# Kernel optimization log

Measured on AMD Instinct MI355X. Metric: run time of the kernel, lower is better.

The kernel has to match this reference:

```python
import jax, jax.numpy as jnp
import numpy as np

N = 4096
IN_DIM = 256
OUT_DIM = 256
E = 131072


def setup_inputs() -> dict:
    key = jax.random.key(0)
    ks = jax.random.split(key, 8)
    x = jax.random.normal(ks[0], (N, IN_DIM), dtype=jnp.float32)
    edge_index = jax.random.randint(ks[1], (2, E), 0, N, dtype=jnp.int64)
    lap = jax.random.normal(ks[2], (N, N), dtype=jnp.float32)
    d_inv = jax.random.normal(ks[3], (N, N), dtype=jnp.float32)
    # parameters
    W_high = jax.random.normal(ks[4], (IN_DIM, OUT_DIM), dtype=jnp.float32) / np.sqrt(IN_DIM)
    W_conv = jax.random.normal(ks[5], (IN_DIM, OUT_DIM), dtype=jnp.float32) / np.sqrt(IN_DIM)
    b_conv = jnp.zeros((OUT_DIM,), dtype=jnp.float32)
    aL = jax.random.uniform(ks[6], (1,), dtype=jnp.float32)
    aH = jax.random.uniform(ks[7], (1,), dtype=jnp.float32)
    return {"x": x, "edge_index": edge_index, "lap": lap, "d_inv": d_inv,
            "W_high": W_high, "W_conv": W_conv, "b_conv": b_conv,
            "aL": aL, "aH": aH}


def _gcn_conv(x, edge_index, W, b, num_nodes):
    # PyG GCNConv: add self-loops, symmetric normalization, aggregate at target.
    src, dst = edge_index[0], edge_index[1]
    loop = jnp.arange(num_nodes, dtype=edge_index.dtype)
    src_f = jnp.concatenate([src, loop])
    dst_f = jnp.concatenate([dst, loop])
    deg = jax.ops.segment_sum(jnp.ones_like(dst_f, dtype=x.dtype), dst_f,
                              num_segments=num_nodes)
    deg_inv_sqrt = jnp.where(deg > 0, jax.lax.rsqrt(jnp.maximum(deg, 1e-12)), 0.0)
    norm = deg_inv_sqrt[src_f] * deg_inv_sqrt[dst_f]  # [E+N]
    xw = x @ W                                        # [N, out]
    msgs = xw[src_f] * norm[:, None]                  # [E+N, out]
    out = jax.ops.segment_sum(msgs, dst_f, num_segments=num_nodes)
    return out + b


def reference(x, edge_index, lap, d_inv, W_high, W_conv, b_conv, aL, aH):
    # high-pass branch: Lhp = d_inv @ lap @ d_inv; Hh = Lhp @ relu(x @ W_high)
    Lhp = (d_inv @ lap) @ d_inv
    Hh = Lhp @ jax.nn.relu(x @ W_high)
    # low-pass branch: GCNConv
    Hl = _gcn_conv(x, edge_index, W_conv, b_conv, x.shape[0])
    return aL * Hl + aH * Hh
```

## Files before the change

### kernel.cpp

```cpp
#include <hip/hip_runtime.h>

#define NN 4096
#define DD 256
#define EE 131072

typedef __attribute__((ext_vector_type(8))) short s16x8;
typedef __attribute__((ext_vector_type(4))) float f32x4;

__device__ __forceinline__ unsigned short f2bf(float f) {
  unsigned u = __builtin_bit_cast(unsigned, f);
  u += 0x7FFFu + ((u >> 16) & 1u);
  return (unsigned short)(u >> 16);
}

__device__ __forceinline__ ushort4 cvt4(f32x4 v) {
  ushort4 r;
  r.x = f2bf(v[0]); r.y = f2bf(v[1]); r.z = f2bf(v[2]); r.w = f2bf(v[3]);
  return r;
}

__device__ __forceinline__ unsigned cvt2_rhu(float a, float b) {
  unsigned ua = __builtin_bit_cast(unsigned, a) + 0x8000u;
  unsigned ub = __builtin_bit_cast(unsigned, b) + 0x8000u;
  return __builtin_amdgcn_perm(ub, ua, 0x07060302u);
}

__device__ __forceinline__ uint4 pack8(f32x4 a, f32x4 b) {
  uint4 r;
  r.x = cvt2_rhu(a[0], a[1]); r.y = cvt2_rhu(a[2], a[3]);
  r.z = cvt2_rhu(b[0], b[1]); r.w = cvt2_rhu(b[2], b[3]);
  return r;
}


__global__ void k_prep(const int* __restrict__ ei, int* __restrict__ deg,
                       const float* __restrict__ Wh, const float* __restrict__ Wc,
                       unsigned short* __restrict__ WFh, unsigned short* __restrict__ WFc) {
  int t = blockIdx.x * 256 + threadIdx.x;
  if (t < EE) {
    atomicAdd(&deg[ei[EE + t]], 1);
  } else {
    int idx = t - EE;
    int which = idx >> 16;
    int r = idx & 65535;
    int n = r & 255, k = r >> 8;
    const float* W = which ? Wc : Wh;
    unsigned short* WF = which ? WFc : WFh;
    long fidx = ((long)((n >> 4) * 8 + (k >> 5))) * 512 +
                (((k >> 3) & 3) * 16 + (n & 15)) * 8 + (k & 7);
    WF[fidx] = f2bf(W[k * 256 + n]);
  }
}

__global__ void k_scan(const int* __restrict__ deg, int* __restrict__ row_start,
                       float* __restrict__ dis) {
  __shared__ int part[1024];
  int t = threadIdx.x;
  int d0 = deg[4 * t + 0], d1 = deg[4 * t + 1], d2 = deg[4 * t + 2], d3 = deg[4 * t + 3];
  int s = d0 + d1 + d2 + d3;
  part[t] = s;
  __syncthreads();
  for (int off = 1; off < 1024; off <<= 1) {
    int add = (t >= off) ? part[t - off] : 0;
    __syncthreads();
    part[t] += add;
    __syncthreads();
  }
  int base = part[t] - s;
  row_start[4 * t + 0] = base;
  row_start[4 * t + 1] = base + d0;
  row_start[4 * t + 2] = base + d0 + d1;
  row_start[4 * t + 3] = base + d0 + d1 + d2;
  if (t == 1023) row_start[4096] = part[t];
  dis[4 * t + 0] = rsqrtf((float)d0 + 1.0f);
  dis[4 * t + 1] = rsqrtf((float)d1 + 1.0f);
  dis[4 * t + 2] = rsqrtf((float)d2 + 1.0f);
  dis[4 * t + 3] = rsqrtf((float)d3 + 1.0f);
}

__global__ void k_scatter(const int* __restrict__ ei, const int* __restrict__ row_start,
                          int* __restrict__ cursor, int* __restrict__ csr) {
  int e = blockIdx.x * 256 + threadIdx.x;
  if (e < EE) {
    int s = ei[e];
    int d = ei[EE + e];
    int p = atomicAdd(&cursor[d], 1);
    csr[row_start[d] + p] = s;
  }
}

__global__ __launch_bounds__(512) void k_xw(const float* __restrict__ x,
                                            const unsigned short* __restrict__ WFh,
                                            const unsigned short* __restrict__ WFc,
                                            unsigned short* __restrict__ RF,
                                            float* __restrict__ XWs,
                                            const float* __restrict__ dis) {
  __shared__ alignas(16) unsigned short Abuf[16][264];
  const int tid = threadIdx.x;
  const int w = tid >> 6, lane = tid & 63;
  const int quad = lane >> 4, l16 = lane & 15, quad8 = quad * 8;
  const int m0 = blockIdx.x * 16;

  {
    int srow = tid >> 5, scolf = (tid & 31) * 8;
    const float* ap = x + (long)(m0 + srow) * DD + scolf;
    f32x4 a0 = *(const f32x4*)ap;
    f32x4 a1 = *(const f32x4*)(ap + 4);
    *(uint4*)&Abuf[srow][scolf] = pack8(a0, a1);
  }
  __syncthreads();

  const bool hi = (w < 4);
  const int wo = hi ? w : (w - 4);
  const unsigned short* WF = hi ? WFh : WFc;
  const unsigned short* bp = WF + lane * 8;

  f32x4 acc[4] = {{0,0,0,0},{0,0,0,0},{0,0,0,0},{0,0,0,0}};
#pragma unroll
  for (int q = 0; q < 8; ++q) {
    s16x8 af = *(const s16x8*)&Abuf[l16][q * 32 + quad8];
#pragma unroll
    for (int s = 0; s < 4; ++s) {
      s16x8 bf = *(const s16x8*)(bp + ((long)((4 * wo + s) * 8 + q)) * 512);
      acc[s] = __builtin_amdgcn_mfma_f32_16x16x32_bf16(af, bf, acc[s], 0, 0, 0);
    }
  }

  if (hi) {
    const int kc = m0 >> 5;
    const int qp = ((m0 >> 4) & 1) * 2 + (quad >> 1);
    const int j0 = (quad & 1) * 4;
#pragma unroll
    for (int s = 0; s < 4; ++s) {
      int t = 4 * wo + s;
      f32x4 v = acc[s];
      f32x4 z;
      z[0] = v[0] > 0.f ? v[0] : 0.f;
      z[1] = v[1] > 0.f ? v[1] : 0.f;
      z[2] = v[2] > 0.f ? v[2] : 0.f;
      z[3] = v[3] > 0.f ? v[3] : 0.f;
      long idx = ((long)(t * 128 + kc)) * 512 + (qp * 16 + l16) * 8 + j0;
      *(ushort4*)(RF + idx) = cvt4(z);
    }
  } else {
    float dm[4];
#pragma unroll
    for (int r = 0; r < 4; ++r) dm[r] = dis[m0 + quad * 4 + r];
#pragma unroll
    for (int s = 0; s < 4; ++s) {
      int col = 64 * wo + 16 * s + l16;
#pragma unroll
      for (int r = 0; r < 4; ++r)
        XWs[(long)(m0 + quad * 4 + r) * DD + col] = dm[r] * acc[s][r];
    }
  }
}

__global__ void k_agg(const float* __restrict__ XWs, const int* __restrict__ row_start,
                      const int* __restrict__ csr, const float* __restrict__ dis,
                      float* __restrict__ Hl) {
  const int i = blockIdx.x;
  const int t = threadIdx.x;
  const int b0 = row_start[i], b1 = row_start[i + 1];
  float acc = XWs[(long)i * DD + t];
  int j = b0;
  for (; j + 4 <= b1; j += 4) {
    int s0 = csr[j], s1 = csr[j + 1], s2 = csr[j + 2], s3 = csr[j + 3];
    float v0 = XWs[(long)s0 * DD + t];
    float v1 = XWs[(long)s1 * DD + t];
    float v2 = XWs[(long)s2 * DD + t];
    float v3 = XWs[(long)s3 * DD + t];
    acc += (v0 + v1) + (v2 + v3);
  }
  for (; j < b1; ++j) acc += XWs[(long)csr[j] * DD + t];
  Hl[(long)i * DD + t] = dis[i] * acc;
}

template <int EPI>
__global__ __launch_bounds__(512) void k_mm2(const float* __restrict__ A,
                                             const unsigned short* __restrict__ BF,
                                             unsigned short* __restrict__ CF,
                                             float* __restrict__ outF,
                                             const float* __restrict__ Hl,
                                             const float* __restrict__ bconv,
                                             const float* __restrict__ aLp,
                                             const float* __restrict__ aHp) {
  __shared__ alignas(16) unsigned short As[2][32 * 512];
  const int tid = threadIdx.x;
  const int w = tid >> 6, lane = tid & 63;
  const int quad = lane >> 4, l16 = lane & 15;
  const int mblk = blockIdx.x & 127, nhalf = blockIdx.x >> 7;
  const int msub = w & 1, nsub = w >> 1;
  const int m0 = mblk * 32;
  const int t0 = nhalf * 8 + nsub * 2;

  const int srow = tid >> 4;
  const int sg = tid & 15;
  const int sswz = srow & 7;
  const float* asrc = A + (long)(m0 + srow) * NN + sg * 8;
  unsigned short* const wbase0 = &As[0][srow * 512];
  unsigned short* const wbase1 = &As[1][srow * 512];

  const int row = msub * 16 + l16;
  const int r7 = row & 7;
  const unsigned short* const rbase0 = &As[0][row * 512];
  const unsigned short* const rbase1 = &As[1][row * 512];

  const unsigned short* bq0 = BF + ((long)t0 * 128) * 512 + lane * 8;
  const unsigned short* bq1 = bq0 + 128l * 512;

  f32x4 acc0 = {0, 0, 0, 0}, acc1 = {0, 0, 0, 0};

  {
#pragma unroll
    for (int j = 0; j < 4; ++j) {
      f32x4 lo = *(const f32x4*)(asrc + j * 128);
      f32x4 hi = *(const f32x4*)(asrc + j * 128 + 4);
      *(uint4*)(wbase0 + (((sg + 16 * j) ^ sswz) * 8)) = pack8(lo, hi);
    }
  }
  __syncthreads();

#pragma unroll 1
  for (int s = 0; s < 8; ++s) {
    f32x4 p0, p1, p2, p3, p4, p5, p6, p7;
    if (s + 1 < 8) {
      const float* ap = asrc + (s + 1) * 512;
      p0 = *(const f32x4*)(ap + 0 * 128); p1 = *(const f32x4*)(ap + 0 * 128 + 4);
      p2 = *(const f32x4*)(ap + 1 * 128); p3 = *(const f32x4*)(ap + 1 * 128 + 4);
      p4 = *(const f32x4*)(ap + 2 * 128); p5 = *(const f32x4*)(ap + 2 * 128 + 4);
      p6 = *(const f32x4*)(ap + 3 * 128); p7 = *(const f32x4*)(ap + 3 * 128 + 4);
    }
    __builtin_amdgcn_sched_barrier(0);

    const unsigned short* rb = (s & 1) ? rbase1 : rbase0;
#pragma unroll
    for (int c = 0; c < 16; ++c) {
      s16x8 af = *(const s16x8*)(rb + (((c * 4 + quad) ^ r7) * 8));
      long kb = (long)(s * 16 + c) * 512;
      s16x8 b0 = *(const s16x8*)(bq0 + kb);
      s16x8 b1 = *(const s16x8*)(bq1 + kb);
      acc0 = __builtin_amdgcn_mfma_f32_16x16x32_bf16(af, b0, acc0, 0, 0, 0);
      acc1 = __builtin_amdgcn_mfma_f32_16x16x32_bf16(af, b1, acc1, 0, 0, 0);
    }

    if (s + 1 < 8) {
      unsigned short* wb = ((s + 1) & 1) ? wbase1 : wbase0;
      *(uint4*)(wb + (((sg + 0)  ^ sswz) * 8)) = pack8(p0, p1);
      *(uint4*)(wb + (((sg + 16) ^ sswz) * 8)) = pack8(p2, p3);
      *(uint4*)(wb + (((sg + 32) ^ sswz) * 8)) = pack8(p4, p5);
      *(uint4*)(wb + (((sg + 48) ^ sswz) * 8)) = pack8(p6, p7);
    }
    __syncthreads();
  }

  if constexpr (EPI == 0) {
    const int qp = msub * 2 + (quad >> 1);
    const int j0 = (quad & 1) * 4;
    long i0 = ((long)(t0 * 128 + mblk)) * 512 + (qp * 16 + l16) * 8 + j0;
    long i1 = ((long)((t0 + 1) * 128 + mblk)) * 512 + (qp * 16 + l16) * 8 + j0;
    *(ushort4*)(CF + i0) = cvt4(acc0);
    *(ushort4*)(CF + i1) = cvt4(acc1);
  } else {
    const float aLv = aLp[0], aHv = aHp[0];
    const int mr = m0 + msub * 16 + quad * 4;
    const int c0 = t0 * 16 + l16;
    const int c1 = c0 + 16;
#pragma unroll
    for (int r = 0; r < 4; ++r) {
      int rr = mr + r;
      outF[(long)rr * DD + c0] =
          aHv * acc0[r] + aLv * (Hl[(long)rr * DD + c0] + bconv[c0]);
      outF[(long)rr * DD + c1] =
          aHv * acc1[r] + aLv * (Hl[(long)rr * DD + c1] + bconv[c1]);
    }
  }
}

extern "C" void kernel_launch(void* const* d_in, const int* in_sizes, int n_in,
                              void* d_out, int out_size, void* d_ws, size_t ws_size,
                              hipStream_t stream) {
  const float* x     = (const float*)d_in[0];
  const int*   ei    = (const int*)d_in[1];
  const float* lap   = (const float*)d_in[2];
  const float* dinv  = (const float*)d_in[3];
  const float* Wh    = (const float*)d_in[4];
  const float* Wc    = (const float*)d_in[5];
  const float* bconv = (const float*)d_in[6];
  const float* aL    = (const float*)d_in[7];
  const float* aH    = (const float*)d_in[8];
  float* out = (float*)d_out;
  char* ws = (char*)d_ws;

  int* deg        = (int*)(ws);
  int* cursor     = (int*)(ws + (16 << 10));
  int* row_start  = (int*)(ws + (32 << 10));
  int* csr        = (int*)(ws + (64 << 10));
  float* dis      = (float*)(ws + (576 << 10));
  unsigned short* WFh = (unsigned short*)(ws + (1l << 20));
  unsigned short* WFc = (unsigned short*)(ws + (1l << 20) + (128 << 10));
  unsigned short* RF  = (unsigned short*)(ws + (2l << 20));
  unsigned short* T1F = (unsigned short*)(ws + (4l << 20));
  unsigned short* T2F = (unsigned short*)(ws + (6l << 20));
  float* XWs = (float*)(ws + (8l << 20));
  float* Hl  = (float*)(ws + (12l << 20));

  hipMemsetAsync(ws, 0, 32 << 10, stream);

  k_prep<<<1024, 256, 0, stream>>>(ei, deg, Wh, Wc, WFh, WFc);
  k_scan<<<1, 1024, 0, stream>>>(deg, row_start, dis);
  k_scatter<<<512, 256, 0, stream>>>(ei, row_start, cursor, csr);
  k_xw<<<256, 512, 0, stream>>>(x, WFh, WFc, RF, XWs, dis);
  k_agg<<<4096, 256, 0, stream>>>(XWs, row_start, csr, dis, Hl);

  k_mm2<0><<<256, 512, 0, stream>>>(dinv, RF, T1F, nullptr, nullptr, nullptr, nullptr, nullptr);
  k_mm2<0><<<256, 512, 0, stream>>>(lap, T1F, T2F, nullptr, nullptr, nullptr, nullptr, nullptr);
  k_mm2<3><<<256, 512, 0, stream>>>(dinv, T2F, nullptr, out, Hl, bconv, aL, aH);
}
```

Baseline: 282.1 us.

## Split-K the big GEMMs with 128-row tiles, async LDS loads, atomic accumulation

Replaces the 32-row-tile GEMM, which read B straight from global memory, with a split-K kernel. Each block handles a 128-row tile over a 512-wide K slice and half of the N columns. A and B are staged into LDS with global_load_lds, and the fp32 A tile is converted to bf16 while building fragments. Partial results are combined with fp32 atomics into a zeroed buffer, and separate convert and finalize kernels write the bf16 fragment layout and the output epilogue. This gives more reuse per block and more parallelism, at the cost of atomic traffic, extra memsets and extra launches.

New measurement: 339.6 us. 1.2x slower.

```diff
diff --git a/kernel.cpp b/kernel.cpp
--- a/kernel.cpp
+++ b/kernel.cpp
@@ -30,6 +30,17 @@
   r.x = cvt2_rhu(a[0], a[1]); r.y = cvt2_rhu(a[2], a[3]);
   r.z = cvt2_rhu(b[0], b[1]); r.w = cvt2_rhu(b[2], b[3]);
   return r;
+}
+
+__device__ __forceinline__ s16x8 pack8f(f32x4 a, f32x4 b) {
+  uint4 p = pack8(a, b);
+  return __builtin_bit_cast(s16x8, p);
+}
+
+__device__ __forceinline__ void gl2lds(const float* g, float* l) {
+  __builtin_amdgcn_global_load_lds(
+      (const __attribute__((address_space(1))) unsigned*)g,
+      (__attribute__((address_space(3))) unsigned*)l, 16, 0, 0);
 }
 
 
@@ -176,105 +187,121 @@
   Hl[(long)i * DD + t] = dis[i] * acc;
 }
 
-template <int EPI>
-__global__ __launch_bounds__(512) void k_mm2(const float* __restrict__ A,
-                                             const unsigned short* __restrict__ BF,
-                                             unsigned short* __restrict__ CF,
-                                             float* __restrict__ outF,
-                                             const float* __restrict__ Hl,
-                                             const float* __restrict__ bconv,
-                                             const float* __restrict__ aLp,
-                                             const float* __restrict__ aHp) {
-  __shared__ alignas(16) unsigned short As[2][32 * 512];
+__global__ __launch_bounds__(256, 3) void k_mm3(const float* __restrict__ A,
+                                                const unsigned short* __restrict__ BF,
+                                                float* __restrict__ C32) {
+  __shared__ alignas(16) float Af[128 * 64];
+  __shared__ alignas(16) unsigned short Bs[8192];
   const int tid = threadIdx.x;
+  const int bid = blockIdx.x;
+  const int mblk = bid >> 4;
+  const int ks = (bid >> 1) & 7;
+  const int h = bid & 1;
+  const int m0 = mblk * 128;
+  const int k0 = ks * 512;
+
   const int w = tid >> 6, lane = tid & 63;
   const int quad = lane >> 4, l16 = lane & 15;
-  const int mblk = blockIdx.x & 127, nhalf = blockIdx.x >> 7;
-  const int msub = w & 1, nsub = w >> 1;
-  const int m0 = mblk * 32;
-  const int t0 = nhalf * 8 + nsub * 2;
-
-  const int srow = tid >> 4;
-  const int sg = tid & 15;
-  const int sswz = srow & 7;
-  const float* asrc = A + (long)(m0 + srow) * NN + sg * 8;
-  unsigned short* const wbase0 = &As[0][srow * 512];
-  unsigned short* const wbase1 = &As[1][srow * 512];
-
-  const int row = msub * 16 + l16;
-  const int r7 = row & 7;
-  const unsigned short* const rbase0 = &As[0][row * 512];
-  const unsigned short* const rbase1 = &As[1][row * 512];
-
-  const unsigned short* bq0 = BF + ((long)t0 * 128) * 512 + lane * 8;
-  const unsigned short* bq1 = bq0 + 128l * 512;
-
-  f32x4 acc0 = {0, 0, 0, 0}, acc1 = {0, 0, 0, 0};
-
-  {
-#pragma unroll
-    for (int j = 0; j < 4; ++j) {
-      f32x4 lo = *(const f32x4*)(asrc + j * 128);
-      f32x4 hi = *(const f32x4*)(asrc + j * 128 + 4);
-      *(uint4*)(wbase0 + (((sg + 16 * j) ^ sswz) * 8)) = pack8(lo, hi);
-    }
-  }
-  __syncthreads();
-
+
+  const int ar = tid >> 4;
+  const int sg = (tid & 15) ^ (ar & 7);
+  const float* asrc = A + (long)(m0 + ar) * NN + k0 + sg * 4;
+  float* adst = Af + tid * 4;
+  const unsigned short* bsrc[4];
+#pragma unroll
+  for (int j = 0; j < 4; ++j) {
+    int gb = tid + 256 * j, ti = gb >> 7, wi = gb & 127;
+    bsrc[j] = BF + ((long)(h * 8 + ti) * 128 + ks * 16) * 512 + wi * 8;
+  }
+  float* bdst = (float*)Bs + tid * 4;
+
+#define STAGE(s)                                                          \
+  {                                                                       \
+    _Pragma("unroll") for (int p = 0; p < 8; ++p)                         \
+        gl2lds(asrc + (long)p * (16 * NN) + (s) * 64, adst + p * 1024);   \
+    _Pragma("unroll") for (int j = 0; j < 4; ++j)                         \
+        gl2lds((const float*)(bsrc[j] + (s) * 1024), bdst + j * 1024);    \
+  }
+
+  f32x4 acc0[8], acc1[8];
+#pragma unroll
+  for (int i = 0; i < 8; ++i) {
+    acc0[i] = (f32x4){0.f, 0.f, 0.f, 0.f};
+    acc1[i] = (f32x4){0.f, 0.f, 0.f, 0.f};
+  }
+
+  const int lr0 = w * 32 + l16;
+  const int xr = l16 & 7;
+  const float* arb0 = Af + lr0 * 64;
+  const float* arb1 = Af + (lr0 + 16) * 64;
+  const unsigned short* bl = Bs + lane * 8;
+
+  STAGE(0);
 #pragma unroll 1
   for (int s = 0; s < 8; ++s) {
-    f32x4 p0, p1, p2, p3, p4, p5, p6, p7;
-    if (s + 1 < 8) {
-      const float* ap = asrc + (s + 1) * 512;
-      p0 = *(const f32x4*)(ap + 0 * 128); p1 = *(const f32x4*)(ap + 0 * 128 + 4);
-      p2 = *(const f32x4*)(ap + 1 * 128); p3 = *(const f32x4*)(ap + 1 * 128 + 4);
-      p4 = *(const f32x4*)(ap + 2 * 128); p5 = *(const f32x4*)(ap + 2 * 128 + 4);
-      p6 = *(const f32x4*)(ap + 3 * 128); p7 = *(const f32x4*)(ap + 3 * 128 + 4);
-    }
-    __builtin_amdgcn_sched_barrier(0);
-
-    const unsigned short* rb = (s & 1) ? rbase1 : rbase0;
-#pragma unroll
-    for (int c = 0; c < 16; ++c) {
-      s16x8 af = *(const s16x8*)(rb + (((c * 4 + quad) ^ r7) * 8));
-      long kb = (long)(s * 16 + c) * 512;
-      s16x8 b0 = *(const s16x8*)(bq0 + kb);
-      s16x8 b1 = *(const s16x8*)(bq1 + kb);
-      acc0 = __builtin_amdgcn_mfma_f32_16x16x32_bf16(af, b0, acc0, 0, 0, 0);
-      acc1 = __builtin_amdgcn_mfma_f32_16x16x32_bf16(af, b1, acc1, 0, 0, 0);
-    }
-
-    if (s + 1 < 8) {
-      unsigned short* wb = ((s + 1) & 1) ? wbase1 : wbase0;
-      *(uint4*)(wb + (((sg + 0)  ^ sswz) * 8)) = pack8(p0, p1);
-      *(uint4*)(wb + (((sg + 16) ^ sswz) * 8)) = pack8(p2, p3);
-      *(uint4*)(wb + (((sg + 32) ^ sswz) * 8)) = pack8(p4, p5);
-      *(uint4*)(wb + (((sg + 48) ^ sswz) * 8)) = pack8(p6, p7);
-    }
     __syncthreads();
-  }
-
-  if constexpr (EPI == 0) {
-    const int qp = msub * 2 + (quad >> 1);
-    const int j0 = (quad & 1) * 4;
-    long i0 = ((long)(t0 * 128 + mblk)) * 512 + (qp * 16 + l16) * 8 + j0;
-    long i1 = ((long)((t0 + 1) * 128 + mblk)) * 512 + (qp * 16 + l16) * 8 + j0;
-    *(ushort4*)(CF + i0) = cvt4(acc0);
-    *(ushort4*)(CF + i1) = cvt4(acc1);
-  } else {
-    const float aLv = aLp[0], aHv = aHp[0];
-    const int mr = m0 + msub * 16 + quad * 4;
-    const int c0 = t0 * 16 + l16;
-    const int c1 = c0 + 16;
+#pragma unroll
+    for (int c = 0; c < 2; ++c) {
+      const int g = c * 8 + quad * 2;
+      f32x4 lo0 = *(const f32x4*)(arb0 + (g ^ xr) * 4);
+      f32x4 hi0 = *(const f32x4*)(arb0 + ((g + 1) ^ xr) * 4);
+      f32x4 lo1 = *(const f32x4*)(arb1 + (g ^ xr) * 4);
+      f32x4 hi1 = *(const f32x4*)(arb1 + ((g + 1) ^ xr) * 4);
+      s16x8 af0 = pack8f(lo0, hi0);
+      s16x8 af1 = pack8f(lo1, hi1);
+#pragma unroll
+      for (int ni = 0; ni < 8; ++ni) {
+        s16x8 bf = *(const s16x8*)(bl + (ni * 2 + c) * 512);
+        acc0[ni] = __builtin_amdgcn_mfma_f32_16x16x32_bf16(af0, bf, acc0[ni], 0, 0, 0);
+        acc1[ni] = __builtin_amdgcn_mfma_f32_16x16x32_bf16(af1, bf, acc1[ni], 0, 0, 0);
+      }
+    }
+    __syncthreads();
+    if (s < 7) STAGE(s + 1);
+  }
+#undef STAGE
+
+  const int grow = m0 + w * 32 + quad * 4;
+  const int gcol = h * 128 + l16;
+#pragma unroll
+  for (int ni = 0; ni < 8; ++ni)
 #pragma unroll
     for (int r = 0; r < 4; ++r) {
-      int rr = mr + r;
-      outF[(long)rr * DD + c0] =
-          aHv * acc0[r] + aLv * (Hl[(long)rr * DD + c0] + bconv[c0]);
-      outF[(long)rr * DD + c1] =
-          aHv * acc1[r] + aLv * (Hl[(long)rr * DD + c1] + bconv[c1]);
-    }
-  }
+      atomicAdd(&C32[(long)(grow + r) * DD + gcol + ni * 16], acc0[ni][r]);
+      atomicAdd(&C32[(long)(grow + 16 + r) * DD + gcol + ni * 16], acc1[ni][r]);
+    }
+}
+
+__global__ void k_cvt(const float* __restrict__ C32, unsigned short* __restrict__ CF) {
+  int t = blockIdx.x * 512 + threadIdx.x;
+  int m = t >> 6;
+  int n4 = (t & 63) * 4;
+  f32x4 v = *(const f32x4*)(C32 + (long)m * DD + n4);
+#pragma unroll
+  for (int j = 0; j < 4; ++j) {
+    int n = n4 + j;
+    long fidx = ((long)((n >> 4) * 128 + (m >> 5))) * 512 +
+                (((m >> 3) & 3) * 16 + (n & 15)) * 8 + (m & 7);
+    CF[fidx] = f2bf(v[j]);
+  }
+}
+
+__global__ void k_fin(const float* __restrict__ C32, const float* __restrict__ Hl,
+                      const float* __restrict__ bconv, const float* __restrict__ aLp,
+                      const float* __restrict__ aHp, float* __restrict__ outF) {
+  int t = blockIdx.x * 512 + threadIdx.x;
+  int m = t >> 6;
+  int n4 = (t & 63) * 4;
+  const float aLv = aLp[0], aHv = aHp[0];
+  f32x4 c = *(const f32x4*)(C32 + (long)m * DD + n4);
+  f32x4 hv = *(const f32x4*)(Hl + (long)m * DD + n4);
+  f32x4 bc = *(const f32x4*)(bconv + n4);
+  f32x4 res;
+  res[0] = aHv * c[0] + aLv * (hv[0] + bc[0]);
+  res[1] = aHv * c[1] + aLv * (hv[1] + bc[1]);
+  res[2] = aHv * c[2] + aLv * (hv[2] + bc[2]);
+  res[3] = aHv * c[3] + aLv * (hv[3] + bc[3]);
+  *(f32x4*)(outF + (long)m * DD + n4) = res;
 }
 
 extern "C" void kernel_launch(void* const* d_in, const int* in_sizes, int n_in,
@@ -303,6 +330,7 @@
   unsigned short* T1F = (unsigned short*)(ws + (4l << 20));
   unsigned short* T2F = (unsigned short*)(ws + (6l << 20));
   float* XWs = (float*)(ws + (8l << 20));
+  float* C32 = (float*)(ws + (8l << 20));
   float* Hl  = (float*)(ws + (12l << 20));
 
   hipMemsetAsync(ws, 0, 32 << 10, stream);
@@ -313,7 +341,13 @@
   k_xw<<<256, 512, 0, stream>>>(x, WFh, WFc, RF, XWs, dis);
   k_agg<<<4096, 256, 0, stream>>>(XWs, row_start, csr, dis, Hl);
 
-  k_mm2<0><<<256, 512, 0, stream>>>(dinv, RF, T1F, nullptr, nullptr, nullptr, nullptr, nullptr);
-  k_mm2<0><<<256, 512, 0, stream>>>(lap, T1F, T2F, nullptr, nullptr, nullptr, nullptr, nullptr);
-  k_mm2<3><<<256, 512, 0, stream>>>(dinv, T2F, nullptr, out, Hl, bconv, aL, aH);
-}
+  hipMemsetAsync(C32, 0, 4 << 20, stream);
+  k_mm3<<<512, 256, 0, stream>>>(dinv, RF, C32);
+  k_cvt<<<512, 512, 0, stream>>>(C32, T1F);
+  hipMemsetAsync(C32, 0, 4 << 20, stream);
+  k_mm3<<<512, 256, 0, stream>>>(lap, T1F, C32);
+  k_cvt<<<512, 512, 0, stream>>>(C32, T2F);
+  hipMemsetAsync(C32, 0, 4 << 20, stream);
+  k_mm3<<<512, 256, 0, stream>>>(dinv, T2F, C32);
+  k_fin<<<512, 512, 0, stream>>>(C32, Hl, bconv, aL, aH, out);
+}
```
